# Kernel optimization log

Measured on AMD Instinct MI355X. Metric: run time of the kernel, lower is better.

The kernel has to match this reference:

```python
import jax, jax.numpy as jnp
from jax import lax
import numpy as np

BATCH, DIM, HID, NSTEPS = 32768, 128, 256, 50

def setup_inputs() -> dict:
    key = jax.random.key(0)
    k1, k2, k3 = jax.random.split(key, 3)
    inputs = jax.random.normal(k1, (BATCH, DIM), dtype=jnp.float32)
    # increasing timestamps over [0, 1] -> 50 Euler steps of dt = 0.02
    timestamps = jnp.linspace(0.0, 1.0, NSTEPS + 1, dtype=jnp.float32)
    # small init keeps the Euler trajectory stable
    W1 = jax.random.normal(k2, (DIM, HID), dtype=jnp.float32) * 0.05
    b1 = jnp.zeros((HID,), dtype=jnp.float32)
    W2 = jax.random.normal(k3, (HID, DIM), dtype=jnp.float32) * 0.05
    b2 = jnp.zeros((DIM,), dtype=jnp.float32)
    return {"inputs": inputs, "timestamps": timestamps, "W1": W1, "b1": b1, "W2": W2, "b2": b2}

def reference(inputs, timestamps, W1, b1, W2, b2):
    """Euler integration of dh/dt = f(h) = tanh(h@W1+b1)@W2+b2; returns final state h(T).
    Matches AdjointODEFunc.forward (which returns states[-1])."""
    dts = timestamps[1:] - timestamps[:-1]  # [NSTEPS]

    def f(h):  # vector field (time-invariant MLP)
        return jnp.tanh(h @ W1 + b1) @ W2 + b2

    def step(h, dt):
        return h + dt * f(h), None

    h_final, _ = lax.scan(step, inputs, dts)
    return h_final
```

## Files before the change

kernel.cpp:

```cpp
#include <hip/hip_runtime.h>


typedef __attribute__((ext_vector_type(8))) short short8;
typedef __attribute__((ext_vector_type(4))) float float4v;
typedef __attribute__((ext_vector_type(4))) int int4v;

union FB { int4v i; short8 s; };

#define W1F_OFF 0
#define W2F_OFF 65536
#define B1_OFF  131072
#define DT_OFF  132096
#define LDS_BYTES 132352

#define TSCALE 2.8853900817779268f

__device__ __forceinline__ unsigned rne2(float x) {
  unsigned u = __float_as_uint(x);
  return u + 0x7fffu + ((u >> 16) & 1u);
}

#if __has_builtin(__builtin_amdgcn_cvt_pk_bf16_f32)
__device__ __forceinline__ int pk2(float lo, float hi) {
  return __builtin_bit_cast(int, __builtin_amdgcn_cvt_pk_bf16_f32(lo, hi));
}
#else
__device__ __forceinline__ int pk2(float lo, float hi) {
  return (int)__builtin_amdgcn_perm(rne2(hi), rne2(lo), 0x07060302u);
}
#endif

__device__ __forceinline__ int4v packfrag(float4v e, float4v o) {
  int4v f;
  f.x = pk2(e.x, e.y);
  f.y = pk2(e.z, e.w);
  f.z = pk2(o.x, o.y);
  f.w = pk2(o.z, o.w);
  return f;
}

#define MFMA16(a, b, c) __builtin_amdgcn_mfma_f32_16x16x32_bf16(a, b, c, 0, 0, 0)

extern "C" __global__ __launch_bounds__(512)
void ode_kernel(const float* __restrict__ inp, const float* __restrict__ ts,
                const float* __restrict__ W1, const float* __restrict__ b1,
                const float* __restrict__ W2, const float* __restrict__ b2,
                float* __restrict__ out) {
  __shared__ __align__(16) char ldsb[LDS_BYTES];
  float* b1f = (float*)(ldsb + B1_OFF);
  float* dtf = (float*)(ldsb + DT_OFF);

  const int tid = threadIdx.x;
  const int lane = tid & 63, wave = tid >> 6;
  const int ln = lane & 15;
  const int q = lane >> 4;
  const int row = blockIdx.x * 128 + wave * 16 + ln;

  #pragma unroll 1
  for (int it = 0; it < 8; it++) {
    const int pi = it * 512 + tid;
    const int fid = pi >> 6, L = pi & 63;
    const int nt = fid >> 2, c = fid & 3;
    const int lf = L & 15, qf = L >> 4;
    const int n = nt * 16 + lf;
    const int kb = c * 32 + qf * 4;
    float v0 = W1[(kb + 0) * 256 + n] * TSCALE;
    float v1 = W1[(kb + 1) * 256 + n] * TSCALE;
    float v2 = W1[(kb + 2) * 256 + n] * TSCALE;
    float v3 = W1[(kb + 3) * 256 + n] * TSCALE;
    float v4 = W1[(kb + 16) * 256 + n] * TSCALE;
    float v5 = W1[(kb + 17) * 256 + n] * TSCALE;
    float v6 = W1[(kb + 18) * 256 + n] * TSCALE;
    float v7 = W1[(kb + 19) * 256 + n] * TSCALE;
    int4v d = {pk2(v0, v1), pk2(v2, v3), pk2(v4, v5), pk2(v6, v7)};
    *(int4v*)(ldsb + W1F_OFF + pi * 16) = d;
  }
  #pragma unroll 1
  for (int it = 0; it < 8; it++) {
    const int pi = it * 512 + tid;
    const int fid = pi >> 6, L = pi & 63;
    const int p = fid >> 3, tb = fid & 7;
    const int lf = L & 15, qf = L >> 4;
    const int d_out = tb * 16 + lf;
    const int kb = p * 32 + qf * 4;
    float v0 = W2[(kb + 0) * 128 + d_out];
    float v1 = W2[(kb + 1) * 128 + d_out];
    float v2 = W2[(kb + 2) * 128 + d_out];
    float v3 = W2[(kb + 3) * 128 + d_out];
    float v4 = W2[(kb + 16) * 128 + d_out];
    float v5 = W2[(kb + 17) * 128 + d_out];
    float v6 = W2[(kb + 18) * 128 + d_out];
    float v7 = W2[(kb + 19) * 128 + d_out];
    int4v d = {pk2(v0, v1), pk2(v2, v3), pk2(v4, v5), pk2(v6, v7)};
    *(int4v*)(ldsb + W2F_OFF + pi * 16) = d;
  }
  if (tid < 256) b1f[tid] = b1[tid] * TSCALE;
  if (tid < 50) dtf[tid] = ts[tid + 1] - ts[tid];

  float4v b2v[8];
  #pragma unroll
  for (int tb = 0; tb < 8; tb++)
    b2v[tb] = *(const float4v*)&b2[tb * 16 + q * 4];

  float4v h4[8];
  #pragma unroll
  for (int tb = 0; tb < 8; tb++)
    h4[tb] = *(const float4v*)&inp[row * 128 + tb * 16 + q * 4];

  __syncthreads();

  const int4v* w1f = (const int4v*)(ldsb + W1F_OFF) + lane;
  const int4v* w2f = (const int4v*)(ldsb + W2F_OFF) + lane;

  #pragma unroll 1
  for (int s = 0; s < 50; s++) {
    const float dt = dtf[s];
    const float m2dt = -2.0f * dt;

    FB hb[4];
    #pragma unroll
    for (int kc = 0; kc < 4; kc++)
      hb[kc].i = packfrag(h4[2 * kc], h4[2 * kc + 1]);

    #pragma unroll 1
    for (int p = 0; p < 8; p++) {
      const int nt0 = 2 * p, nt1 = 2 * p + 1;
      FB wA[4], wB[4];
      #pragma unroll
      for (int c = 0; c < 4; c++) {
        wA[c].i = w1f[(nt0 * 4 + c) * 64];
        wB[c].i = w1f[(nt1 * 4 + c) * 64];
      }
      float4v g0 = *(const float4v*)&b1f[nt0 * 16 + q * 4];
      float4v g1 = *(const float4v*)&b1f[nt1 * 16 + q * 4];
      #pragma unroll
      for (int c = 0; c < 4; c++) {
        g0 = MFMA16(wA[c].s, hb[c].s, g0);
        g1 = MFMA16(wB[c].s, hb[c].s, g1);
      }

      FB w2r[8];
      #pragma unroll
      for (int tb = 0; tb < 8; tb++)
        w2r[tb].i = w2f[(p * 8 + tb) * 64];

      float4v a0, a1;
      #pragma unroll
      for (int r = 0; r < 4; r++) {
        a0[r] = fmaf(__builtin_amdgcn_rcpf(__builtin_amdgcn_exp2f(g0[r]) + 1.0f), m2dt, dt);
        a1[r] = fmaf(__builtin_amdgcn_rcpf(__builtin_amdgcn_exp2f(g1[r]) + 1.0f), m2dt, dt);
      }
      FB af;
      af.i = packfrag(a0, a1);

      #pragma unroll
      for (int tb = 0; tb < 8; tb++)
        h4[tb] = MFMA16(w2r[tb].s, af.s, h4[tb]);
    }

    #pragma unroll
    for (int tb = 0; tb < 8; tb++)
      #pragma unroll
      for (int r = 0; r < 4; r++)
        h4[tb][r] = fmaf(dt, b2v[tb][r], h4[tb][r]);
  }

  #pragma unroll
  for (int tb = 0; tb < 8; tb++)
    *(float4v*)&out[row * 128 + tb * 16 + q * 4] = h4[tb];
}

extern "C" void kernel_launch(void* const* d_in, const int* in_sizes, int n_in,
                              void* d_out, int out_size, void* d_ws, size_t ws_size,
                              hipStream_t stream) {
  const float* inp = (const float*)d_in[0];
  const float* ts  = (const float*)d_in[1];
  const float* W1  = (const float*)d_in[2];
  const float* b1  = (const float*)d_in[3];
  const float* W2  = (const float*)d_in[4];
  const float* b2  = (const float*)d_in[5];
  hipLaunchKernelGGL(ode_kernel, dim3(256), dim3(512), 0, stream,
                     inp, ts, W1, b1, W2, b2, (float*)d_out);
}
```

Baseline: 316.7 us.

## Software-pipeline hidden-chunk loop so second GEMM overlaps activation math

Restructures the per-step loop over hidden chunks into prologue, steady state and epilogue. The layer-2 MFMAs for chunk p-1 are now issued between the layer-1 MFMAs and the tanh math for chunk p, so matrix and transcendental work can overlap within a wave. It also adds a minimum of two blocks per CU to launch_bounds, which caps registers per thread. The LDS use of about 132 KB per block may still allow only one block per CU, so that cap could force spills without raising occupancy.

```diff
diff --git a/kernel.cpp b/kernel.cpp
--- a/kernel.cpp
+++ b/kernel.cpp
@@ -41,7 +41,7 @@
 
 #define MFMA16(a, b, c) __builtin_amdgcn_mfma_f32_16x16x32_bf16(a, b, c, 0, 0, 0)
 
-extern "C" __global__ __launch_bounds__(512)
+extern "C" __global__ __launch_bounds__(512, 2)
 void ode_kernel(const float* __restrict__ inp, const float* __restrict__ ts,
                 const float* __restrict__ W1, const float* __restrict__ b1,
                 const float* __restrict__ W2, const float* __restrict__ b2,
@@ -122,37 +122,69 @@
     for (int kc = 0; kc < 4; kc++)
       hb[kc].i = packfrag(h4[2 * kc], h4[2 * kc + 1]);
 
-    #pragma unroll 1
-    for (int p = 0; p < 8; p++) {
-      const int nt0 = 2 * p, nt1 = 2 * p + 1;
+    FB af;
+    {
       FB wA[4], wB[4];
       #pragma unroll
       for (int c = 0; c < 4; c++) {
-        wA[c].i = w1f[(nt0 * 4 + c) * 64];
-        wB[c].i = w1f[(nt1 * 4 + c) * 64];
-      }
-      float4v g0 = *(const float4v*)&b1f[nt0 * 16 + q * 4];
-      float4v g1 = *(const float4v*)&b1f[nt1 * 16 + q * 4];
+        wA[c].i = w1f[(0 * 4 + c) * 64];
+        wB[c].i = w1f[(1 * 4 + c) * 64];
+      }
+      float4v g0 = *(const float4v*)&b1f[0 * 16 + q * 4];
+      float4v g1 = *(const float4v*)&b1f[1 * 16 + q * 4];
       #pragma unroll
       for (int c = 0; c < 4; c++) {
         g0 = MFMA16(wA[c].s, hb[c].s, g0);
         g1 = MFMA16(wB[c].s, hb[c].s, g1);
       }
-
-      FB w2r[8];
-      #pragma unroll
-      for (int tb = 0; tb < 8; tb++)
-        w2r[tb].i = w2f[(p * 8 + tb) * 64];
-
       float4v a0, a1;
       #pragma unroll
       for (int r = 0; r < 4; r++) {
         a0[r] = fmaf(__builtin_amdgcn_rcpf(__builtin_amdgcn_exp2f(g0[r]) + 1.0f), m2dt, dt);
         a1[r] = fmaf(__builtin_amdgcn_rcpf(__builtin_amdgcn_exp2f(g1[r]) + 1.0f), m2dt, dt);
       }
-      FB af;
       af.i = packfrag(a0, a1);
-
+    }
+
+    #pragma unroll 1
+    for (int p = 1; p < 8; p++) {
+      const int nt0 = 2 * p, nt1 = 2 * p + 1;
+      FB wA[4], wB[4];
+      #pragma unroll
+      for (int c = 0; c < 4; c++) {
+        wA[c].i = w1f[(nt0 * 4 + c) * 64];
+        wB[c].i = w1f[(nt1 * 4 + c) * 64];
+      }
+      float4v g0 = *(const float4v*)&b1f[nt0 * 16 + q * 4];
+      float4v g1 = *(const float4v*)&b1f[nt1 * 16 + q * 4];
+      #pragma unroll
+      for (int c = 0; c < 4; c++) {
+        g0 = MFMA16(wA[c].s, hb[c].s, g0);
+        g1 = MFMA16(wB[c].s, hb[c].s, g1);
+      }
+      {
+        FB w2r[8];
+        #pragma unroll
+        for (int tb = 0; tb < 8; tb++)
+          w2r[tb].i = w2f[((p - 1) * 8 + tb) * 64];
+        #pragma unroll
+        for (int tb = 0; tb < 8; tb++)
+          h4[tb] = MFMA16(w2r[tb].s, af.s, h4[tb]);
+      }
+      float4v a0, a1;
+      #pragma unroll
+      for (int r = 0; r < 4; r++) {
+        a0[r] = fmaf(__builtin_amdgcn_rcpf(__builtin_amdgcn_exp2f(g0[r]) + 1.0f), m2dt, dt);
+        a1[r] = fmaf(__builtin_amdgcn_rcpf(__builtin_amdgcn_exp2f(g1[r]) + 1.0f), m2dt, dt);
+      }
+      af.i = packfrag(a0, a1);
+    }
+
+    {
+      FB w2r[8];
+      #pragma unroll
+      for (int tb = 0; tb < 8; tb++)
+        w2r[tb].i = w2f[(7 * 8 + tb) * 64];
       #pragma unroll
       for (int tb = 0; tb < 8; tb++)
         h4[tb] = MFMA16(w2r[tb].s, af.s, h4[tb]);
```

Measured after the change: 310.4 us. 1.02x faster.
